# Optimization experiments

Hardware: AMD Instinct MI355X
Metric: run time of the kernel (lower is better)

The kernel has to match this reference:

```python
import jax, jax.numpy as jnp
import numpy as np

N_NODES, N_EDGES, N_GRAPHS = 50000, 800000, 128
D_IN, D_DEG, D_H, D_OUT, MAX_DEG = 32, 32, 64, 32, 128
D0 = D_IN + D_DEG + 1  # 65 = node_input_dim
N_GIN = 5  # num_layers - 1


def setup_inputs() -> dict:
    key = jax.random.key(0)
    ks = jax.random.split(key, 20)
    lin = lambda k, i, o: (jax.random.normal(k, (i, o), jnp.float32) / np.sqrt(i)).astype(jnp.float32)
    inp = {
        "x": jax.random.normal(ks[0], (N_NODES, D_IN), jnp.float32),
        "edge_index": jax.random.randint(ks[1], (2, N_EDGES), 0, N_NODES, jnp.int32),
        "batch": jnp.sort(jax.random.randint(ks[2], (N_NODES,), 0, N_GRAPHS, jnp.int32)),
        "root_n_id": jax.random.randint(ks[3], (N_GRAPHS,), 0, N_NODES, jnp.int32),
        "deg_table": 0.1 * jax.random.normal(ks[4], (MAX_DEG + 1, D_DEG), jnp.float32),
        # GIN layer 0 MLP (input dim 65), layers 1..4 (input dim 64), each MLP has 2 linears
        "w1_0": lin(ks[5], D0, D_H), "b1_0": 0.01 * jax.random.normal(ks[6], (D_H,), jnp.float32),
        "w2_0": lin(ks[7], D_H, D_H), "b2_0": 0.01 * jax.random.normal(ks[8], (D_H,), jnp.float32),
        "w1_rest": jnp.stack([lin(jax.random.fold_in(ks[9], i), D_H, D_H) for i in range(N_GIN - 1)]),
        "b1_rest": 0.01 * jax.random.normal(ks[10], (N_GIN - 1, D_H), jnp.float32),
        "w2_rest": jnp.stack([lin(jax.random.fold_in(ks[11], i), D_H, D_H) for i in range(N_GIN - 1)]),
        "b2_rest": 0.01 * jax.random.normal(ks[12], (N_GIN - 1, D_H), jnp.float32),
        # 3 BatchNorms per GIN layer: MLP-hidden BN, ApplyNodeFunc BN, outer BN
        "bn_gamma": 1.0 + 0.1 * jax.random.normal(ks[13], (N_GIN, 3, D_H), jnp.float32),
        "bn_beta": 0.1 * jax.random.normal(ks[14], (N_GIN, 3, D_H), jnp.float32),
        # per-layer prediction heads (layer 0 sees raw n_feat of dim 65)
        "pred_w0": lin(ks[15], D0, D_OUT), "pred_b0": 0.01 * jax.random.normal(ks[16], (D_OUT,), jnp.float32),
        "pred_w_rest": jnp.stack([lin(jax.random.fold_in(ks[17], i), D_H, D_OUT) for i in range(N_GIN)]),
        "pred_b_rest": 0.01 * jax.random.normal(ks[18], (N_GIN, D_OUT), jnp.float32),
    }
    return inp


def _bn(h, g, b):
    # training-mode BatchNorm1d over the node axis (biased variance), eps=1e-5
    m = h.mean(axis=0)
    v = h.var(axis=0)
    return g * (h - m) * jax.lax.rsqrt(v + 1e-5) + b


def _forward(x, edge_index, batch, root_n_id, deg_table, w1_0, b1_0, w2_0, b2_0,
             w1_rest, b1_rest, w2_rest, b2_rest, bn_gamma, bn_beta,
             pred_w0, pred_b0, pred_w_rest, pred_b_rest):
    N = x.shape[0]
    G = root_n_id.shape[0]
    src, dst = edge_index[0], edge_index[1]

    # degree(edge_index[0]) clamped to max_degree, then embedded
    deg = jax.ops.segment_sum(jnp.ones_like(src), src, num_segments=N)
    deg = jnp.clip(deg, 0, deg_table.shape[0] - 1)
    ego = jnp.zeros((N, 1), x.dtype).at[root_n_id].set(1.0)
    h = jnp.concatenate([x, deg_table[deg], ego], axis=-1)  # [N, 65]

    w1s = [w1_0] + [w1_rest[i] for i in range(w1_rest.shape[0])]
    b1s = [b1_0] + [b1_rest[i] for i in range(b1_rest.shape[0])]
    w2s = [w2_0] + [w2_rest[i] for i in range(w2_rest.shape[0])]
    b2s = [b2_0] + [b2_rest[i] for i in range(b2_rest.shape[0])]

    hidden = [h]
    for l in range(len(w1s)):
        # GINConv, sum aggregation, eps = 0: (1+eps)*h + sum_{j in N(i)} h_j
        agg = jax.ops.segment_sum(h[src], dst, num_segments=N)  # [N, d]
        z = h + agg
        z = jax.nn.relu(_bn(z @ w1s[l] + b1s[l], bn_gamma[l, 0], bn_beta[l, 0]))  # MLP hidden
        z = z @ w2s[l] + b2s[l]                                                  # MLP out (linear)
        z = jax.nn.relu(_bn(z, bn_gamma[l, 1], bn_beta[l, 1]))                   # ApplyNodeFunc BN+ReLU
        z = jax.nn.relu(_bn(z, bn_gamma[l, 2], bn_beta[l, 2]))                   # outer BN+ReLU
        h = z
        hidden.append(h)

    pred_ws = [pred_w0] + [pred_w_rest[i] for i in range(pred_w_rest.shape[0])]
    pred_bs = [pred_b0] + [pred_b_rest[i] for i in range(pred_b_rest.shape[0])]
    score = jnp.zeros((G, pred_w0.shape[1]), x.dtype)
    for i, hi in enumerate(hidden):
        pooled = jax.ops.segment_sum(hi, batch, num_segments=G)  # global_add_pool
        score = score + pooled @ pred_ws[i] + pred_bs[i]         # dropout is identity in eval
    # F.normalize(p=2, eps=1e-5)
    nrm = jnp.maximum(jnp.linalg.norm(score, axis=-1, keepdims=True), 1e-5)
    return score / nrm


def reference(x, edge_index, batch, root_n_id, deg_table, w1_0, b1_0, w2_0, b2_0,
              w1_rest, b1_rest, w2_rest, b2_rest, bn_gamma, bn_beta,
              pred_w0, pred_b0, pred_w_rest, pred_b_rest):
    return _forward(x, edge_index, batch, root_n_id, deg_table, w1_0, b1_0, w2_0, b2_0,
                    w1_rest, b1_rest, w2_rest, b2_rest, bn_gamma, bn_beta,
                    pred_w0, pred_b0, pred_w_rest, pred_b_rest)
```

## Files before the change

### kernel.cpp

```cpp
#include <hip/hip_runtime.h>
#include <hip/hip_fp16.h>

#define PAD 8
#define NREP 16
#define CHUNK 64

#define BCAST(v, l) __uint_as_float(__builtin_amdgcn_readlane(__float_as_uint(v), (l)))

__global__ __launch_bounds__(256) void count_k(const int* __restrict__ src,
    const int* __restrict__ dst, int* __restrict__ deg, int* __restrict__ cnt, int E) {
  int e = blockIdx.x * 256 + threadIdx.x;
  if (e < E) {
    atomicAdd(&deg[src[e] * PAD], 1);
    atomicAdd(&cnt[dst[e] * PAD], 1);
  }
}

__global__ __launch_bounds__(256) void scan1_k(const int* __restrict__ cnt,
    int* __restrict__ off, int* __restrict__ bsum, int N) {
  __shared__ int s[256];
  int t = threadIdx.x;
  int i = blockIdx.x * 256 + t;
  int c = (i < N) ? cnt[i * PAD] : 0;
  s[t] = c;
  __syncthreads();
  for (int d = 1; d < 256; d <<= 1) {
    int v = (t >= d) ? s[t - d] : 0;
    __syncthreads();
    s[t] += v;
    __syncthreads();
  }
  if (i < N) off[i + 1] = s[t];
  if (t == 255) bsum[blockIdx.x] = s[255];
}

__global__ __launch_bounds__(256) void scan2root_k(int* __restrict__ bsum, int NB,
    const int* __restrict__ root, int* __restrict__ egof, int G) {
  __shared__ int s[256];
  int t = threadIdx.x;
  if (t < G) egof[root[t]] = 1;
  int c = (t < NB) ? bsum[t] : 0;
  s[t] = c;
  __syncthreads();
  for (int d = 1; d < 256; d <<= 1) {
    int v = (t >= d) ? s[t - d] : 0;
    __syncthreads();
    s[t] += v;
    __syncthreads();
  }
  if (t < NB) bsum[t] = s[t] - c;
}

__global__ __launch_bounds__(256) void scan3_k(int* __restrict__ off,
    const int* __restrict__ bsum, int N) {
  int i = blockIdx.x * 256 + threadIdx.x;
  if (i < N) off[i + 1] += bsum[blockIdx.x];
  if (i == 0) off[0] = 0;
}

__global__ __launch_bounds__(256) void fillh0_k(const int* __restrict__ src,
    const int* __restrict__ dst, const int* __restrict__ off, int* __restrict__ cnt,
    int* __restrict__ csr, int E, const float* __restrict__ x,
    const float* __restrict__ deg_table, const int* __restrict__ deg,
    const int* __restrict__ egof, const int* __restrict__ batch,
    __half* __restrict__ h0, float* __restrict__ pool0, int N, int ebl) {
  if ((int)blockIdx.x < ebl) {
    int e = blockIdx.x * 256 + threadIdx.x;
    if (e < E) {
      int d = dst[e];
      int old = atomicSub(&cnt[d * PAD], 1);
      csr[off[d + 1] - old] = src[e];
    }
    return;
  }
  int bid = blockIdx.x - ebl;
  int w = threadIdx.x >> 6, f = threadIdx.x & 63;
  int base = bid * CHUNK;
  int end = min(base + CHUNK, N);
  float accum = 0.0f, accum64 = 0.0f;
  int curg = -1;
  for (int n0 = base + w; n0 < end; n0 += 4) {
    int n = __builtin_amdgcn_readfirstlane(n0);
    float v;
    if (f < 32) {
      v = x[n * 32 + f];
    } else {
      int d = deg[n * PAD];
      if (d > 128) d = 128;
      v = deg_table[d * 32 + (f - 32)];
    }
    __half vh = __float2half(v);
    v = __half2float(vh);
    h0[(size_t)n * 72 + f] = vh;
    float e = 0.0f;
    if (f == 0) {
      e = egof[n] ? 1.0f : 0.0f;
      h0[(size_t)n * 72 + 64] = __float2half(e);
    }
    int g = batch[n];
    if (g != curg) {
      if (curg >= 0) {
        atomicAdd(&pool0[curg * 72 + f], accum);
        if (f == 0 && accum64 != 0.0f) atomicAdd(&pool0[curg * 72 + 64], accum64);
      }
      curg = g;
      accum = v;
      accum64 = e;
    } else {
      accum += v;
      accum64 += e;
    }
  }
  if (curg >= 0) {
    atomicAdd(&pool0[curg * 72 + f], accum);
    if (f == 0 && accum64 != 0.0f) atomicAdd(&pool0[curg * 72 + 64], accum64);
  }
}

template <int FEATS, int STRIDE>
__global__ __launch_bounds__(256) void layer1_k(const __half* __restrict__ h,
    const int* __restrict__ off, const int* __restrict__ csr,
    const float* __restrict__ W1, const float* __restrict__ B1,
    float* __restrict__ z1, float* __restrict__ sums, int N) {
  __shared__ float Wsh[FEATS * 64];
  __shared__ float ls[256], lq[256];
  const int t = threadIdx.x;
  for (int i = t; i < FEATS * 64; i += 256) Wsh[i] = W1[i];
  __syncthreads();
  const int w = t >> 6, lane = t & 63;
  const float bj = B1[lane];
  float s = 0.0f, q = 0.0f;
  const int step = gridDim.x * 4;
  for (int n0 = blockIdx.x * 4 + w; n0 < N; n0 += step) {
    const int n = __builtin_amdgcn_readfirstlane(n0);
    const __half* row = h + (size_t)n * STRIDE;
    float z = __half2float(row[lane]);
    float z64 = 0.0f;
    if (FEATS == 65) { if (lane == 0) z64 = __half2float(row[64]); }
    const int k1 = off[n + 1];
    int k = off[n];
    for (; k + 8 <= k1; k += 8) {
      int i0 = csr[k], i1 = csr[k + 1], i2 = csr[k + 2], i3 = csr[k + 3];
      int i4 = csr[k + 4], i5 = csr[k + 5], i6 = csr[k + 6], i7 = csr[k + 7];
      const __half* r0 = h + (size_t)i0 * STRIDE;
      const __half* r1 = h + (size_t)i1 * STRIDE;
      const __half* r2 = h + (size_t)i2 * STRIDE;
      const __half* r3 = h + (size_t)i3 * STRIDE;
      const __half* r4 = h + (size_t)i4 * STRIDE;
      const __half* r5 = h + (size_t)i5 * STRIDE;
      const __half* r6 = h + (size_t)i6 * STRIDE;
      const __half* r7 = h + (size_t)i7 * STRIDE;
      float v0 = __half2float(r0[lane]), v1 = __half2float(r1[lane]);
      float v2 = __half2float(r2[lane]), v3 = __half2float(r3[lane]);
      float v4 = __half2float(r4[lane]), v5 = __half2float(r5[lane]);
      float v6 = __half2float(r6[lane]), v7 = __half2float(r7[lane]);
      if (FEATS == 65) {
        if (lane == 0)
          z64 += ((__half2float(r0[64]) + __half2float(r1[64])) +
                  (__half2float(r2[64]) + __half2float(r3[64]))) +
                 ((__half2float(r4[64]) + __half2float(r5[64])) +
                  (__half2float(r6[64]) + __half2float(r7[64])));
      }
      z += ((v0 + v1) + (v2 + v3)) + ((v4 + v5) + (v6 + v7));
    }
    for (; k < k1; k++) {
      const __half* r0 = h + (size_t)csr[k] * STRIDE;
      z += __half2float(r0[lane]);
      if (FEATS == 65) { if (lane == 0) z64 += __half2float(r0[64]); }
    }
    float a0 = bj, a1 = 0.0f, a2 = 0.0f, a3 = 0.0f;
#pragma unroll
    for (int k2 = 0; k2 < 64; k2 += 4) {
      a0 += BCAST(z, k2) * Wsh[k2 * 64 + lane];
      a1 += BCAST(z, k2 + 1) * Wsh[(k2 + 1) * 64 + lane];
      a2 += BCAST(z, k2 + 2) * Wsh[(k2 + 2) * 64 + lane];
      a3 += BCAST(z, k2 + 3) * Wsh[(k2 + 3) * 64 + lane];
    }
    if (FEATS == 65) a0 += BCAST(z64, 0) * Wsh[64 * 64 + lane];
    float acc = (a0 + a1) + (a2 + a3);
    z1[(size_t)n * 64 + lane] = acc;
    s += acc;
    q += acc * acc;
  }
  ls[t] = s; lq[t] = q;
  __syncthreads();
  if (t < 64) {
    float a = ls[t] + ls[64 + t] + ls[128 + t] + ls[192 + t];
    atomicAdd(&sums[(blockIdx.x & (NREP - 1)) * 128 + t], a);
  } else if (t < 128) {
    int f = t - 64;
    float a = lq[f] + lq[64 + f] + lq[128 + f] + lq[192 + f];
    atomicAdd(&sums[(blockIdx.x & (NREP - 1)) * 128 + 64 + f], a);
  }
}

__global__ __launch_bounds__(512) void layer2_k(const float* __restrict__ z1,
    const float* __restrict__ W2, const float* __restrict__ B2,
    const float* __restrict__ sums0, const float* __restrict__ g0,
    const float* __restrict__ be0, float invN,
    float* __restrict__ z2, float* __restrict__ sums1, int N) {
  __shared__ float Wsh[64 * 64];
  __shared__ float redu[128];
  __shared__ float scs[64], shs[64];
  __shared__ float ls[512], lq[512];
  const int t = threadIdx.x;
  for (int i = t; i < 64 * 64; i += 512) Wsh[i] = W2[i];
  if (t < 128) {
    float a = 0.0f;
#pragma unroll
    for (int b = 0; b < NREP; b++) a += sums0[b * 128 + t];
    redu[t] = a;
  }
  __syncthreads();
  if (t < 64) {
    float m = redu[t] * invN;
    float var = redu[64 + t] * invN - m * m;
    float sc = g0[t] * rsqrtf(var + 1e-5f);
    scs[t] = sc;
    shs[t] = be0[t] - m * sc;
  }
  __syncthreads();
  const int w = t >> 6, lane = t & 63;
  const float sc = scs[lane], sh = shs[lane];
  const float bj = B2[lane];
  float s = 0.0f, q = 0.0f;
  const int step = gridDim.x * 8;
  for (int n0 = blockIdx.x * 8 + w; n0 < N; n0 += step) {
    const int n = __builtin_amdgcn_readfirstlane(n0);
    float v = z1[(size_t)n * 64 + lane];
    v = fmaxf(v * sc + sh, 0.0f);
    float a0 = bj, a1 = 0.0f, a2 = 0.0f, a3 = 0.0f;
#pragma unroll
    for (int k2 = 0; k2 < 64; k2 += 4) {
      a0 += BCAST(v, k2) * Wsh[k2 * 64 + lane];
      a1 += BCAST(v, k2 + 1) * Wsh[(k2 + 1) * 64 + lane];
      a2 += BCAST(v, k2 + 2) * Wsh[(k2 + 2) * 64 + lane];
      a3 += BCAST(v, k2 + 3) * Wsh[(k2 + 3) * 64 + lane];
    }
    float acc = (a0 + a1) + (a2 + a3);
    z2[(size_t)n * 64 + lane] = acc;
    s += acc;
    q += acc * acc;
  }
  ls[t] = s;
  lq[t] = q;
  __syncthreads();
  if (t < 64) {
    float a = 0.0f;
#pragma unroll
    for (int r = 0; r < 8; r++) a += ls[r * 64 + t];
    atomicAdd(&sums1[(blockIdx.x & (NREP - 1)) * 128 + t], a);
  } else if (t < 128) {
    int f = t - 64;
    float a = 0.0f;
#pragma unroll
    for (int r = 0; r < 8; r++) a += lq[r * 64 + f];
    atomicAdd(&sums1[(blockIdx.x & (NREP - 1)) * 128 + 64 + f], a);
  }
}

__global__ __launch_bounds__(1024) void statsbn_k(const float* __restrict__ z2,
    const float* __restrict__ sums1, const float* __restrict__ g1,
    const float* __restrict__ be1, float invN, float* __restrict__ sums2, int N) {
  __shared__ float redu[128];
  __shared__ float scs[64], shs[64];
  __shared__ float ls[1024], lq[1024];
  int t = threadIdx.x;
  if (t < 128) {
    float a = 0.0f;
#pragma unroll
    for (int b = 0; b < NREP; b++) a += sums1[b * 128 + t];
    redu[t] = a;
  }
  __syncthreads();
  if (t < 64) {
    float m = redu[t] * invN;
    float var = redu[64 + t] * invN - m * m;
    float sc = g1[t] * rsqrtf(var + 1e-5f);
    scs[t] = sc;
    shs[t] = be1[t] - m * sc;
  }
  __syncthreads();
  int f = t & 63, r = t >> 6;
  float sc = scs[f], sh = shs[f];
  float s = 0.0f, q = 0.0f;
  for (int n = blockIdx.x * 16 + r; n < N; n += gridDim.x * 16) {
    float v = z2[(size_t)n * 64 + f];
    v = fmaxf(v * sc + sh, 0.0f);
    s += v;
    q += v * v;
  }
  ls[t] = s;
  lq[t] = q;
  __syncthreads();
  if (t < 64) {
    float a = 0.0f;
#pragma unroll
    for (int rr = 0; rr < 16; rr++) a += ls[rr * 64 + t];
    atomicAdd(&sums2[(blockIdx.x & (NREP - 1)) * 128 + t], a);
  } else if (t < 128) {
    int ff = t - 64;
    float a = 0.0f;
#pragma unroll
    for (int rr = 0; rr < 16; rr++) a += lq[rr * 64 + ff];
    atomicAdd(&sums2[(blockIdx.x & (NREP - 1)) * 128 + 64 + ff], a);
  }
}

__global__ __launch_bounds__(256) void apply_k(const float* __restrict__ z2,
    const float* __restrict__ sums1, const float* __restrict__ g1, const float* __restrict__ be1,
    const float* __restrict__ sums2, const float* __restrict__ g2, const float* __restrict__ be2,
    float invN, const int* __restrict__ batch, __half* __restrict__ hout,
    float* __restrict__ pool, int N, int writeH) {
  __shared__ float red1[128], red2[128];
  __shared__ float sc1s[64], sh1s[64], sc2s[64], sh2s[64];
  int t = threadIdx.x;
  if (t < 128) {
    float a = 0.0f, c = 0.0f;
#pragma unroll
    for (int b = 0; b < NREP; b++) { a += sums1[b * 128 + t]; c += sums2[b * 128 + t]; }
    red1[t] = a;
    red2[t] = c;
  }
  __syncthreads();
  if (t < 64) {
    float m = red1[t] * invN;
    float var = red1[64 + t] * invN - m * m;
    float sc = g1[t] * rsqrtf(var + 1e-5f);
    sc1s[t] = sc;
    sh1s[t] = be1[t] - m * sc;
    m = red2[t] * invN;
    var = red2[64 + t] * invN - m * m;
    sc = g2[t] * rsqrtf(var + 1e-5f);
    sc2s[t] = sc;
    sh2s[t] = be2[t] - m * sc;
  }
  __syncthreads();
  int w = t >> 6, f = t & 63;
  float sc1 = sc1s[f], sh1 = sh1s[f], sc2 = sc2s[f], sh2 = sh2s[f];
  int base = blockIdx.x * CHUNK;
  int end = min(base + CHUNK, N);
  float accum = 0.0f;
  int curg = -1;
  for (int n0 = base + w; n0 < end; n0 += 4) {
    int n = __builtin_amdgcn_readfirstlane(n0);
    float v = z2[(size_t)n * 64 + f];
    v = fmaxf(v * sc1 + sh1, 0.0f);
    v = fmaxf(v * sc2 + sh2, 0.0f);
    __half vh = __float2half(v);
    v = __half2float(vh);
    if (writeH) hout[(size_t)n * 64 + f] = vh;
    int g = batch[n];
    if (g != curg) {
      if (curg >= 0) atomicAdd(&pool[curg * 64 + f], accum);
      curg = g;
      accum = v;
    } else {
      accum += v;
    }
  }
  if (curg >= 0) atomicAdd(&pool[curg * 64 + f], accum);
}

__global__ __launch_bounds__(64) void prednorm_k(const float* __restrict__ pool0,
    const float* __restrict__ pools, const float* __restrict__ pw0,
    const float* __restrict__ pb0, const float* __restrict__ pwr,
    const float* __restrict__ pbr, float* __restrict__ out, int G) {
  int g = blockIdx.x;
  int j = threadIdx.x;
  float acc = 0.0f;
  if (j < 32) {
    acc = pb0[j];
    for (int k = 0; k < 65; k++) acc += pool0[g * 72 + k] * pw0[k * 32 + j];
    for (int l = 0; l < 5; l++) {
      acc += pbr[l * 32 + j];
      const float* pl = pools + (size_t)l * G * 64 + (size_t)g * 64;
      const float* wl = pwr + (size_t)l * 64 * 32;
      for (int k = 0; k < 64; k++) acc += pl[k] * wl[k * 32 + j];
    }
  }
  float s = acc * acc;
  for (int o = 16; o > 0; o >>= 1) s += __shfl_xor(s, o);
  float nrm = fmaxf(sqrtf(s), 1e-5f);
  if (j < 32) out[g * 32 + j] = acc / nrm;
}

extern "C" void kernel_launch(void* const* d_in, const int* in_sizes, int n_in,
                              void* d_out, int out_size, void* d_ws, size_t ws_size,
                              hipStream_t stream) {
  (void)n_in; (void)out_size; (void)ws_size;
  const float* x          = (const float*)d_in[0];
  const int*   edge_index = (const int*)d_in[1];
  const int*   batch      = (const int*)d_in[2];
  const int*   root       = (const int*)d_in[3];
  const float* deg_table  = (const float*)d_in[4];
  const float* w1_0       = (const float*)d_in[5];
  const float* b1_0       = (const float*)d_in[6];
  const float* w2_0       = (const float*)d_in[7];
  const float* b2_0       = (const float*)d_in[8];
  const float* w1_rest    = (const float*)d_in[9];
  const float* b1_rest    = (const float*)d_in[10];
  const float* w2_rest    = (const float*)d_in[11];
  const float* b2_rest    = (const float*)d_in[12];
  const float* bn_gamma   = (const float*)d_in[13];
  const float* bn_beta    = (const float*)d_in[14];
  const float* pred_w0    = (const float*)d_in[15];
  const float* pred_b0    = (const float*)d_in[16];
  const float* pred_w_rest = (const float*)d_in[17];
  const float* pred_b_rest = (const float*)d_in[18];

  const int N = in_sizes[0] / 32;
  const int E = in_sizes[1] / 2;
  const int G = in_sizes[3];
  const int* src = edge_index;
  const int* dst = edge_index + E;
  const float invN = 1.0f / N;

  char* w = (char*)d_ws;
  auto alloc = [&](size_t bytes) {
    char* p = w;
    w += (bytes + 255) & ~(size_t)255;
    return p;
  };
  int* d_deg  = (int*)alloc((size_t)N * PAD * 4);
  int* d_cnt  = (int*)alloc((size_t)N * PAD * 4);
  int* d_egof = (int*)alloc((size_t)N * 4);
  char* zero_int_end = w;
  int* d_off  = (int*)alloc((size_t)(N + 1) * 4);
  int* d_bsum = (int*)alloc(256 * 4);
  int* d_csr  = (int*)alloc((size_t)E * 4);
  float* fsums = (float*)alloc((size_t)15 * NREP * 128 * 4);
  float* fpool = (float*)alloc((size_t)(G * 72 + 5 * G * 64) * 4);
  char* zero_f_end = w;
  __half* fh0 = (__half*)alloc((size_t)N * 72 * 2);
  __half* fH  = (__half*)alloc((size_t)N * 64 * 2);
  __half* fH2 = (__half*)alloc((size_t)N * 64 * 2);
  float* fB1 = (float*)alloc((size_t)N * 64 * 4);
  float* fB2 = (float*)alloc((size_t)N * 64 * 4);

  hipMemsetAsync(d_deg, 0, (size_t)(zero_int_end - (char*)d_deg), stream);
  hipMemsetAsync(fsums, 0, (size_t)(zero_f_end - (char*)fsums), stream);

  const int ebl = (E + 255) / 256;
  const int nb  = (N + 255) / 256;
  const int ncb = (N + CHUNK - 1) / CHUNK;

  count_k<<<ebl, 256, 0, stream>>>(src, dst, d_deg, d_cnt, E);
  scan1_k<<<nb, 256, 0, stream>>>(d_cnt, d_off, d_bsum, N);
  scan2root_k<<<1, 256, 0, stream>>>(d_bsum, nb, root, d_egof, G);
  scan3_k<<<nb, 256, 0, stream>>>(d_off, d_bsum, N);
  fillh0_k<<<ebl + ncb, 256, 0, stream>>>(src, dst, d_off, d_cnt, d_csr, E,
      x, deg_table, d_deg, d_egof, batch, fh0, fpool, N, ebl);

  float* pools = fpool + G * 72;
  const __half* hcur = fh0;
  __half* hnext = fH;
  for (int l = 0; l < 5; l++) {
    const float* w1 = (l == 0) ? w1_0 : w1_rest + (size_t)(l - 1) * 64 * 64;
    const float* b1 = (l == 0) ? b1_0 : b1_rest + (size_t)(l - 1) * 64;
    const float* w2 = (l == 0) ? w2_0 : w2_rest + (size_t)(l - 1) * 64 * 64;
    const float* b2 = (l == 0) ? b2_0 : b2_rest + (size_t)(l - 1) * 64;
    float* sums0 = fsums + (size_t)(l * 3 + 0) * NREP * 128;
    float* sums1 = fsums + (size_t)(l * 3 + 1) * NREP * 128;
    float* sums2 = fsums + (size_t)(l * 3 + 2) * NREP * 128;
    const float* g0 = bn_gamma + (l * 3 + 0) * 64;
    const float* be0 = bn_beta + (l * 3 + 0) * 64;
    const float* g1 = bn_gamma + (l * 3 + 1) * 64;
    const float* be1 = bn_beta + (l * 3 + 1) * 64;
    const float* g2 = bn_gamma + (l * 3 + 2) * 64;
    const float* be2 = bn_beta + (l * 3 + 2) * 64;

    if (l == 0)
      layer1_k<65, 72><<<2048, 256, 0, stream>>>(hcur, d_off, d_csr, w1, b1, fB1, sums0, N);
    else
      layer1_k<64, 64><<<2048, 256, 0, stream>>>(hcur, d_off, d_csr, w1, b1, fB1, sums0, N);
    layer2_k<<<1024, 512, 0, stream>>>(fB1, w2, b2, sums0, g0, be0, invN, fB2, sums1, N);
    statsbn_k<<<512, 1024, 0, stream>>>(fB2, sums1, g1, be1, invN, sums2, N);
    float* pool_l = pools + (size_t)l * G * 64;
    apply_k<<<ncb, 256, 0, stream>>>(fB2, sums1, g1, be1, sums2, g2, be2, invN,
                                     batch, hnext, pool_l, N, (l < 4) ? 1 : 0);
    hcur = hnext;
    hnext = (hnext == fH) ? fH2 : fH;
  }
  prednorm_k<<<G, 64, 0, stream>>>(fpool, pools, pred_w0, pred_b0,
                                   pred_w_rest, pred_b_rest, (float*)d_out, G);
}
```

Baseline: 638.2 us.

## Store intermediate MLP activations in fp16 and widen neighbor gather unroll

Result: faster. 612.1 us (-4.1%).

```diff
diff --git a/kernel.cpp b/kernel.cpp
--- a/kernel.cpp
+++ b/kernel.cpp
@@ -121,7 +121,7 @@
 __global__ __launch_bounds__(256) void layer1_k(const __half* __restrict__ h,
     const int* __restrict__ off, const int* __restrict__ csr,
     const float* __restrict__ W1, const float* __restrict__ B1,
-    float* __restrict__ z1, float* __restrict__ sums, int N) {
+    __half* __restrict__ z1, float* __restrict__ sums, int N) {
   __shared__ float Wsh[FEATS * 64];
   __shared__ float ls[256], lq[256];
   const int t = threadIdx.x;
@@ -139,29 +139,39 @@
     if (FEATS == 65) { if (lane == 0) z64 = __half2float(row[64]); }
     const int k1 = off[n + 1];
     int k = off[n];
-    for (; k + 8 <= k1; k += 8) {
+    for (; k + 16 <= k1; k += 16) {
+      int idx[16];
+#pragma unroll
+      for (int j = 0; j < 16; j++) idx[j] = csr[k + j];
+      float v[16];
+#pragma unroll
+      for (int j = 0; j < 16; j++)
+        v[j] = __half2float(h[(size_t)idx[j] * STRIDE + lane]);
+      if (FEATS == 65) {
+        if (lane == 0) {
+#pragma unroll
+          for (int j = 0; j < 16; j++)
+            z64 += __half2float(h[(size_t)idx[j] * STRIDE + 64]);
+        }
+      }
+      float t0 = ((v[0] + v[1]) + (v[2] + v[3])) + ((v[4] + v[5]) + (v[6] + v[7]));
+      float t1 = ((v[8] + v[9]) + (v[10] + v[11])) + ((v[12] + v[13]) + (v[14] + v[15]));
+      z += t0 + t1;
+    }
+    for (; k + 4 <= k1; k += 4) {
       int i0 = csr[k], i1 = csr[k + 1], i2 = csr[k + 2], i3 = csr[k + 3];
-      int i4 = csr[k + 4], i5 = csr[k + 5], i6 = csr[k + 6], i7 = csr[k + 7];
-      const __half* r0 = h + (size_t)i0 * STRIDE;
-      const __half* r1 = h + (size_t)i1 * STRIDE;
-      const __half* r2 = h + (size_t)i2 * STRIDE;
-      const __half* r3 = h + (size_t)i3 * STRIDE;
-      const __half* r4 = h + (size_t)i4 * STRIDE;
-      const __half* r5 = h + (size_t)i5 * STRIDE;
-      const __half* r6 = h + (size_t)i6 * STRIDE;
-      const __half* r7 = h + (size_t)i7 * STRIDE;
-      float v0 = __half2float(r0[lane]), v1 = __half2float(r1[lane]);
-      float v2 = __half2float(r2[lane]), v3 = __half2float(r3[lane]);
-      float v4 = __half2float(r4[lane]), v5 = __half2float(r5[lane]);
-      float v6 = __half2float(r6[lane]), v7 = __half2float(r7[lane]);
+      float v0 = __half2float(h[(size_t)i0 * STRIDE + lane]);
+      float v1 = __half2float(h[(size_t)i1 * STRIDE + lane]);
+      float v2 = __half2float(h[(size_t)i2 * STRIDE + lane]);
+      float v3 = __half2float(h[(size_t)i3 * STRIDE + lane]);
       if (FEATS == 65) {
         if (lane == 0)
-          z64 += ((__half2float(r0[64]) + __half2float(r1[64])) +
-                  (__half2float(r2[64]) + __half2float(r3[64]))) +
-                 ((__half2float(r4[64]) + __half2float(r5[64])) +
-                  (__half2float(r6[64]) + __half2float(r7[64])));
+          z64 += (__half2float(h[(size_t)i0 * STRIDE + 64]) +
+                  __half2float(h[(size_t)i1 * STRIDE + 64])) +
+                 (__half2float(h[(size_t)i2 * STRIDE + 64]) +
+                  __half2float(h[(size_t)i3 * STRIDE + 64]));
       }
-      z += ((v0 + v1) + (v2 + v3)) + ((v4 + v5) + (v6 + v7));
+      z += (v0 + v1) + (v2 + v3);
     }
     for (; k < k1; k++) {
       const __half* r0 = h + (size_t)csr[k] * STRIDE;
@@ -178,9 +188,11 @@
     }
     if (FEATS == 65) a0 += BCAST(z64, 0) * Wsh[64 * 64 + lane];
     float acc = (a0 + a1) + (a2 + a3);
-    z1[(size_t)n * 64 + lane] = acc;
-    s += acc;
-    q += acc * acc;
+    __half ah = __float2half(acc);
+    float accr = __half2float(ah);
+    z1[(size_t)n * 64 + lane] = ah;
+    s += accr;
+    q += accr * accr;
   }
   ls[t] = s; lq[t] = q;
   __syncthreads();
@@ -194,11 +206,11 @@
   }
 }
 
-__global__ __launch_bounds__(512) void layer2_k(const float* __restrict__ z1,
+__global__ __launch_bounds__(512) void layer2_k(const __half* __restrict__ z1,
     const float* __restrict__ W2, const float* __restrict__ B2,
     const float* __restrict__ sums0, const float* __restrict__ g0,
     const float* __restrict__ be0, float invN,
-    float* __restrict__ z2, float* __restrict__ sums1, int N) {
+    __half* __restrict__ z2, float* __restrict__ sums1, int N) {
   __shared__ float Wsh[64 * 64];
   __shared__ float redu[128];
   __shared__ float scs[64], shs[64];
@@ -227,7 +239,7 @@
   const int step = gridDim.x * 8;
   for (int n0 = blockIdx.x * 8 + w; n0 < N; n0 += step) {
     const int n = __builtin_amdgcn_readfirstlane(n0);
-    float v = z1[(size_t)n * 64 + lane];
+    float v = __half2float(z1[(size_t)n * 64 + lane]);
     v = fmaxf(v * sc + sh, 0.0f);
     float a0 = bj, a1 = 0.0f, a2 = 0.0f, a3 = 0.0f;
 #pragma unroll
@@ -238,9 +250,11 @@
       a3 += BCAST(v, k2 + 3) * Wsh[(k2 + 3) * 64 + lane];
     }
     float acc = (a0 + a1) + (a2 + a3);
-    z2[(size_t)n * 64 + lane] = acc;
-    s += acc;
-    q += acc * acc;
+    __half ah = __float2half(acc);
+    float accr = __half2float(ah);
+    z2[(size_t)n * 64 + lane] = ah;
+    s += accr;
+    q += accr * accr;
   }
   ls[t] = s;
   lq[t] = q;
@@ -259,7 +273,7 @@
   }
 }
 
-__global__ __launch_bounds__(1024) void statsbn_k(const float* __restrict__ z2,
+__global__ __launch_bounds__(1024) void statsbn_k(const __half* __restrict__ z2,
     const float* __restrict__ sums1, const float* __restrict__ g1,
     const float* __restrict__ be1, float invN, float* __restrict__ sums2, int N) {
   __shared__ float redu[128];
@@ -285,7 +299,7 @@
   float sc = scs[f], sh = shs[f];
   float s = 0.0f, q = 0.0f;
   for (int n = blockIdx.x * 16 + r; n < N; n += gridDim.x * 16) {
-    float v = z2[(size_t)n * 64 + f];
+    float v = __half2float(z2[(size_t)n * 64 + f]);
     v = fmaxf(v * sc + sh, 0.0f);
     s += v;
     q += v * v;
@@ -307,7 +321,7 @@
   }
 }
 
-__global__ __launch_bounds__(256) void apply_k(const float* __restrict__ z2,
+__global__ __launch_bounds__(256) void apply_k(const __half* __restrict__ z2,
     const float* __restrict__ sums1, const float* __restrict__ g1, const float* __restrict__ be1,
     const float* __restrict__ sums2, const float* __restrict__ g2, const float* __restrict__ be2,
     float invN, const int* __restrict__ batch, __half* __restrict__ hout,
@@ -344,7 +358,7 @@
   int curg = -1;
   for (int n0 = base + w; n0 < end; n0 += 4) {
     int n = __builtin_amdgcn_readfirstlane(n0);
-    float v = z2[(size_t)n * 64 + f];
+    float v = __half2float(z2[(size_t)n * 64 + f]);
     v = fmaxf(v * sc1 + sh1, 0.0f);
     v = fmaxf(v * sc2 + sh2, 0.0f);
     __half vh = __float2half(v);
@@ -435,8 +449,8 @@
   __half* fh0 = (__half*)alloc((size_t)N * 72 * 2);
   __half* fH  = (__half*)alloc((size_t)N * 64 * 2);
   __half* fH2 = (__half*)alloc((size_t)N * 64 * 2);
-  float* fB1 = (float*)alloc((size_t)N * 64 * 4);
-  float* fB2 = (float*)alloc((size_t)N * 64 * 4);
+  __half* fB1 = (__half*)alloc((size_t)N * 64 * 2);
+  __half* fB2 = (__half*)alloc((size_t)N * 64 * 2);
 
   hipMemsetAsync(d_deg, 0, (size_t)(zero_int_end - (char*)d_deg), stream);
   hipMemsetAsync(fsums, 0, (size_t)(zero_f_end - (char*)fsums), stream);
```
